# Kernel tuning notes

Hardware: AMD Instinct MI355X
Metric: run time of the kernel (lower is better)

Reference implementation:

```python
import jax, jax.numpy as jnp
import numpy as np

H = 64  # hidden_layers

def _lstm_cell(x, h, c, Wih, Whh, bih, bhh):
    # PyTorch LSTMCell: gates ordered i, f, g, o
    gates = x @ Wih.T + bih + h @ Whh.T + bhh  # (B, 4H)
    i, f, g, o = jnp.split(gates, 4, axis=-1)
    c_new = jax.nn.sigmoid(f) * c + jax.nn.sigmoid(i) * jnp.tanh(g)
    h_new = jax.nn.sigmoid(o) * jnp.tanh(c_new)
    return h_new, c_new

def setup_inputs() -> dict:
    key = jax.random.key(0)
    ks = jax.random.split(key, 12)
    B, S = 1024, 512
    s1 = 1.0 / np.sqrt(H)
    u = lambda k, shape: jax.random.uniform(k, shape, jnp.float32, -s1, s1)
    return {
        "input_t": jax.random.normal(ks[0], (B, S), jnp.float32),
        "W_ih1": u(ks[1], (4 * H, 1)),
        "W_hh1": u(ks[2], (4 * H, H)),
        "b_ih1": u(ks[3], (4 * H,)),
        "b_hh1": u(ks[4], (4 * H,)),
        "W_ih2": u(ks[5], (4 * H, H)),
        "W_hh2": u(ks[6], (4 * H, H)),
        "b_ih2": u(ks[7], (4 * H,)),
        "b_hh2": u(ks[8], (4 * H,)),
        "W_lin": u(ks[9], (1, H)),
        "b_lin": u(ks[10], (1,)),
        "future_preds": 0,
    }

def reference(input_t, W_ih1, W_hh1, b_ih1, b_hh1, W_ih2, W_hh2, b_ih2, b_hh2,
              W_lin, b_lin, future_preds):
    B = input_t.shape[0]
    z = jnp.zeros((B, H), jnp.float32)

    def step(carry, x_t):
        h1, c1, h2, c2 = carry
        h1, c1 = _lstm_cell(x_t, h1, c1, W_ih1, W_hh1, b_ih1, b_hh1)
        h2, c2 = _lstm_cell(h1, h2, c2, W_ih2, W_hh2, b_ih2, b_hh2)
        out = h2 @ W_lin.T + b_lin  # (B, 1)
        return (h1, c1, h2, c2), out[:, 0]

    xs = input_t.T[:, :, None]  # (S, B, 1)
    carry, outs = jax.lax.scan(step, (z, z, z, z), xs)
    outputs = outs.T  # (B, S)

    if future_preds > 0:  # static Python int
        def step_ar(carry_o, _):
            (h1, c1, h2, c2), out = carry_o
            h1, c1 = _lstm_cell(out, h1, c1, W_ih1, W_hh1, b_ih1, b_hh1)
            h2, c2 = _lstm_cell(h1, h2, c2, W_ih2, W_hh2, b_ih2, b_hh2)
            out = h2 @ W_lin.T + b_lin
            return ((h1, c1, h2, c2), out), out[:, 0]

        last = outs[-1][:, None]  # (B, 1)
        _, outs2 = jax.lax.scan(step_ar, (carry, last), None, length=future_preds)
        outputs = jnp.concatenate([outputs, outs2.T], axis=1)
    return outputs
```

## Files before the change

kernel.cpp:

```cpp
#include <hip/hip_runtime.h>
#include <stdint.h>

#define HD   64
#define SEQ  512
#define BTCH 1024

typedef _Float16 half2_t __attribute__((ext_vector_type(2)));

static __device__ __forceinline__ float fdot2f(uint32_t w, uint32_t hv, float acc) {
#if __has_builtin(__builtin_amdgcn_fdot2)
    half2_t a = __builtin_bit_cast(half2_t, w);
    half2_t b = __builtin_bit_cast(half2_t, hv);
    return __builtin_amdgcn_fdot2(a, b, acc, false);
#else
    half2_t a = __builtin_bit_cast(half2_t, w);
    half2_t b = __builtin_bit_cast(half2_t, hv);
    return acc + (float)a[0] * (float)b[0] + (float)a[1] * (float)b[1];
#endif
}

static __device__ __forceinline__ float rcpf_(float x) {
#if __has_builtin(__builtin_amdgcn_rcpf)
    return __builtin_amdgcn_rcpf(x);
#else
    return 1.0f / x;
#endif
}

static __device__ __forceinline__ float sigmoidf_(float x) {
    return rcpf_(1.0f + __expf(-x));
}
static __device__ __forceinline__ float tanhf_(float x) {
    float e = __expf(2.0f * x);
    return (e - 1.0f) * rcpf_(e + 1.0f);
}

static __device__ __forceinline__ uint32_t pack2h(float a, float b) {
    _Float16 ha = (_Float16)a, hb = (_Float16)b;
    uint16_t ua = __builtin_bit_cast(uint16_t, ha);
    uint16_t ub = __builtin_bit_cast(uint16_t, hb);
    return (uint32_t)ua | ((uint32_t)ub << 16);
}

static __device__ __forceinline__ uint16_t f2h(float a) {
    _Float16 ha = (_Float16)a;
    return __builtin_bit_cast(uint16_t, ha);
}

__global__ __attribute__((amdgpu_flat_work_group_size(128, 128),
                          amdgpu_waves_per_eu(2, 2)))
void lstm_kernel(
    const float* __restrict__ input,
    const float* __restrict__ Wih1,
    const float* __restrict__ Whh1,
    const float* __restrict__ bih1,
    const float* __restrict__ bhh1,
    const float* __restrict__ Wih2,
    const float* __restrict__ Whh2,
    const float* __restrict__ bih2,
    const float* __restrict__ bhh2,
    const float* __restrict__ Wlin,
    const float* __restrict__ blin,
    float* __restrict__ out)
{
    const int tid  = threadIdx.x;
    const int lane = tid & 63;
    const int gg   = tid >> 6;
    const int b    = blockIdx.x;

    const int r0 = gg * 128 + lane;
    const int r1 = r0 + 64;

    uint32_t w1a[32], w1b[32], wi2a[32], wi2b[32], wh2a[32], wh2b[32];
#pragma unroll
    for (int k = 0; k < 32; ++k) {
        w1a[k]  = pack2h(Whh1[r0 * HD + 2 * k], Whh1[r0 * HD + 2 * k + 1]);
        w1b[k]  = pack2h(Whh1[r1 * HD + 2 * k], Whh1[r1 * HD + 2 * k + 1]);
        wi2a[k] = pack2h(Wih2[r0 * HD + 2 * k], Wih2[r0 * HD + 2 * k + 1]);
        wi2b[k] = pack2h(Wih2[r1 * HD + 2 * k], Wih2[r1 * HD + 2 * k + 1]);
        wh2a[k] = pack2h(Whh2[r0 * HD + 2 * k], Whh2[r0 * HD + 2 * k + 1]);
        wh2b[k] = pack2h(Whh2[r1 * HD + 2 * k], Whh2[r1 * HD + 2 * k + 1]);
    }
    const float wx0  = Wih1[r0];
    const float wx1  = Wih1[r1];
    const float bs10 = bih1[r0] + bhh1[r0];
    const float bs11 = bih1[r1] + bhh1[r1];
    const float bs20 = bih2[r0] + bhh2[r0];
    const float bs21 = bih2[r1] + bhh2[r1];
    const float wl   = Wlin[lane];
    const float bl   = blin[0];

    __shared__ __align__(16) uint16_t hp1[2][HD];
    __shared__ __align__(16) uint16_t hp2[2][HD];
    __shared__ float g1x[4][HD];
    __shared__ float g2x[4][HD];

    hp1[gg][lane] = 0;
    hp2[gg][lane] = 0;

    float h1 = 0.f, c1 = 0.f, h2 = 0.f, c2 = 0.f;

    const float* xin = input + (size_t)b * SEQ;
    float xn = xin[0];

#pragma unroll 1
    for (int t = 0; t < SEQ; ++t) {
        const float x = xn;
        xn = xin[(t + 1) & (SEQ - 1)];

        float a0  = __builtin_fmaf(x, wx0, bs10);
        float a1  = __builtin_fmaf(x, wx1, bs11);
        float a0b = 0.f, a1b = 0.f;
        {
            const uint4* h1v = (const uint4*)(&hp1[gg][0]);
#pragma unroll
            for (int k = 0; k < 8; ++k) {
                uint4 hv = h1v[k];
                a0  = fdot2f(w1a[4 * k + 0], hv.x, a0);
                a0b = fdot2f(w1a[4 * k + 1], hv.y, a0b);
                a0  = fdot2f(w1a[4 * k + 2], hv.z, a0);
                a0b = fdot2f(w1a[4 * k + 3], hv.w, a0b);
                a1  = fdot2f(w1b[4 * k + 0], hv.x, a1);
                a1b = fdot2f(w1b[4 * k + 1], hv.y, a1b);
                a1  = fdot2f(w1b[4 * k + 2], hv.z, a1);
                a1b = fdot2f(w1b[4 * k + 3], hv.w, a1b);
            }
        }
        a0 += a0b;
        a1 += a1b;
        g1x[2 * gg + 0][lane] = a0;
        g1x[2 * gg + 1][lane] = a1;
        __syncthreads();

        {
            const float gi = gg ? g1x[0][lane] : a0;
            const float gf = gg ? g1x[1][lane] : a1;
            const float gG = gg ? a0 : g1x[2][lane];
            const float gO = gg ? a1 : g1x[3][lane];
            c1 = sigmoidf_(gf) * c1 + sigmoidf_(gi) * tanhf_(gG);
            h1 = sigmoidf_(gO) * tanhf_(c1);
        }
        hp1[gg][lane] = f2h(h1);

        float d0  = bs20;
        float d1  = bs21;
        float d0b = 0.f, d1b = 0.f;
        {
            const uint4* h1v = (const uint4*)(&hp1[gg][0]);
            const uint4* h2v = (const uint4*)(&hp2[gg][0]);
#pragma unroll
            for (int k = 0; k < 8; ++k) {
                uint4 hv = h1v[k];
                d0  = fdot2f(wi2a[4 * k + 0], hv.x, d0);
                d0b = fdot2f(wi2a[4 * k + 1], hv.y, d0b);
                d0  = fdot2f(wi2a[4 * k + 2], hv.z, d0);
                d0b = fdot2f(wi2a[4 * k + 3], hv.w, d0b);
                d1  = fdot2f(wi2b[4 * k + 0], hv.x, d1);
                d1b = fdot2f(wi2b[4 * k + 1], hv.y, d1b);
                d1  = fdot2f(wi2b[4 * k + 2], hv.z, d1);
                d1b = fdot2f(wi2b[4 * k + 3], hv.w, d1b);
                uint4 hw = h2v[k];
                d0  = fdot2f(wh2a[4 * k + 0], hw.x, d0);
                d0b = fdot2f(wh2a[4 * k + 1], hw.y, d0b);
                d0  = fdot2f(wh2a[4 * k + 2], hw.z, d0);
                d0b = fdot2f(wh2a[4 * k + 3], hw.w, d0b);
                d1  = fdot2f(wh2b[4 * k + 0], hw.x, d1);
                d1b = fdot2f(wh2b[4 * k + 1], hw.y, d1b);
                d1  = fdot2f(wh2b[4 * k + 2], hw.z, d1);
                d1b = fdot2f(wh2b[4 * k + 3], hw.w, d1b);
            }
        }
        d0 += d0b;
        d1 += d1b;
        g2x[2 * gg + 0][lane] = d0;
        g2x[2 * gg + 1][lane] = d1;
        __syncthreads();

        {
            const float gi = gg ? g2x[0][lane] : d0;
            const float gf = gg ? g2x[1][lane] : d1;
            const float gG = gg ? d0 : g2x[2][lane];
            const float gO = gg ? d1 : g2x[3][lane];
            c2 = sigmoidf_(gf) * c2 + sigmoidf_(gi) * tanhf_(gG);
            h2 = sigmoidf_(gO) * tanhf_(c2);
        }
        hp2[gg][lane] = f2h(h2);

        float r = h2 * wl;
#pragma unroll
        for (int m = 32; m >= 1; m >>= 1) r += __shfl_xor(r, m, 64);
        if (gg == 0 && lane == 0) out[(size_t)b * SEQ + t] = r + bl;
    }
}

extern "C" void kernel_launch(void* const* d_in, const int* in_sizes, int n_in,
                              void* d_out, int out_size, void* d_ws, size_t ws_size,
                              hipStream_t stream) {
    const float* input = (const float*)d_in[0];
    const float* Wih1  = (const float*)d_in[1];
    const float* Whh1  = (const float*)d_in[2];
    const float* bih1  = (const float*)d_in[3];
    const float* bhh1  = (const float*)d_in[4];
    const float* Wih2  = (const float*)d_in[5];
    const float* Whh2  = (const float*)d_in[6];
    const float* bih2  = (const float*)d_in[7];
    const float* bhh2  = (const float*)d_in[8];
    const float* Wlin  = (const float*)d_in[9];
    const float* blin  = (const float*)d_in[10];

    float* outp = (float*)d_out;

    lstm_kernel<<<dim3(BTCH), dim3(128), 0, stream>>>(
        input, Wih1, Whh1, bih1, bhh1, Wih2, Whh2, bih2, bhh2, Wlin, blin, outp);
}
```

Measured before the change: 917.0 us.

## Use four waves per block with one gate row per lane

Moves from 2 waves per block, each computing two gate rows per lane, to 4 waves per block with one gate row per lane. Each wave now does half the dot-product work per step and holds half the weight registers, which shortens the serial per-step chain and allows higher occupancy (waves_per_eu 4). In exchange, every wave redundantly computes the full cell update for all 64 hidden units. More waves also share each barrier, and the register budget per wave is tighter.

```diff
diff --git a/kernel.cpp b/kernel.cpp
--- a/kernel.cpp
+++ b/kernel.cpp
@@ -47,8 +47,8 @@
     return __builtin_bit_cast(uint16_t, ha);
 }
 
-__global__ __attribute__((amdgpu_flat_work_group_size(128, 128),
-                          amdgpu_waves_per_eu(2, 2)))
+__global__ __attribute__((amdgpu_flat_work_group_size(256, 256),
+                          amdgpu_waves_per_eu(4, 4)))
 void lstm_kernel(
     const float* __restrict__ input,
     const float* __restrict__ Wih1,
@@ -65,40 +65,33 @@
 {
     const int tid  = threadIdx.x;
     const int lane = tid & 63;
-    const int gg   = tid >> 6;
+    const int g    = tid >> 6;
     const int b    = blockIdx.x;
 
-    const int r0 = gg * 128 + lane;
-    const int r1 = r0 + 64;
+    const int row = g * HD + lane;
 
-    uint32_t w1a[32], w1b[32], wi2a[32], wi2b[32], wh2a[32], wh2b[32];
+    uint32_t w1[32], wi2[32], wh2[32];
 #pragma unroll
     for (int k = 0; k < 32; ++k) {
-        w1a[k]  = pack2h(Whh1[r0 * HD + 2 * k], Whh1[r0 * HD + 2 * k + 1]);
-        w1b[k]  = pack2h(Whh1[r1 * HD + 2 * k], Whh1[r1 * HD + 2 * k + 1]);
-        wi2a[k] = pack2h(Wih2[r0 * HD + 2 * k], Wih2[r0 * HD + 2 * k + 1]);
-        wi2b[k] = pack2h(Wih2[r1 * HD + 2 * k], Wih2[r1 * HD + 2 * k + 1]);
-        wh2a[k] = pack2h(Whh2[r0 * HD + 2 * k], Whh2[r0 * HD + 2 * k + 1]);
-        wh2b[k] = pack2h(Whh2[r1 * HD + 2 * k], Whh2[r1 * HD + 2 * k + 1]);
+        w1[k]  = pack2h(Whh1[row * HD + 2 * k], Whh1[row * HD + 2 * k + 1]);
+        wi2[k] = pack2h(Wih2[row * HD + 2 * k], Wih2[row * HD + 2 * k + 1]);
+        wh2[k] = pack2h(Whh2[row * HD + 2 * k], Whh2[row * HD + 2 * k + 1]);
     }
-    const float wx0  = Wih1[r0];
-    const float wx1  = Wih1[r1];
-    const float bs10 = bih1[r0] + bhh1[r0];
-    const float bs11 = bih1[r1] + bhh1[r1];
-    const float bs20 = bih2[r0] + bhh2[r0];
-    const float bs21 = bih2[r1] + bhh2[r1];
-    const float wl   = Wlin[lane];
-    const float bl   = blin[0];
+    const float wx  = Wih1[row];
+    const float bs1 = bih1[row] + bhh1[row];
+    const float bs2 = bih2[row] + bhh2[row];
+    const float wl  = Wlin[lane];
+    const float bl  = blin[0];
 
-    __shared__ __align__(16) uint16_t hp1[2][HD];
-    __shared__ __align__(16) uint16_t hp2[2][HD];
+    __shared__ __align__(16) uint16_t hp1[4][HD];
+    __shared__ __align__(16) uint16_t hp2[4][HD];
     __shared__ float g1x[4][HD];
     __shared__ float g2x[4][HD];
 
-    hp1[gg][lane] = 0;
-    hp2[gg][lane] = 0;
+    hp1[g][lane] = 0;
+    hp2[g][lane] = 0;
 
-    float h1 = 0.f, c1 = 0.f, h2 = 0.f, c2 = 0.f;
+    float c1 = 0.f, c2 = 0.f;
 
     const float* xin = input + (size_t)b * SEQ;
     float xn = xin[0];
@@ -108,88 +101,74 @@
         const float x = xn;
         xn = xin[(t + 1) & (SEQ - 1)];
 
-        float a0  = __builtin_fmaf(x, wx0, bs10);
-        float a1  = __builtin_fmaf(x, wx1, bs11);
-        float a0b = 0.f, a1b = 0.f;
+        float a0  = __builtin_fmaf(x, wx, bs1);
+        float a0b = 0.f;
         {
-            const uint4* h1v = (const uint4*)(&hp1[gg][0]);
+            const uint4* h1v = (const uint4*)(&hp1[g][0]);
 #pragma unroll
             for (int k = 0; k < 8; ++k) {
                 uint4 hv = h1v[k];
-                a0  = fdot2f(w1a[4 * k + 0], hv.x, a0);
-                a0b = fdot2f(w1a[4 * k + 1], hv.y, a0b);
-                a0  = fdot2f(w1a[4 * k + 2], hv.z, a0);
-                a0b = fdot2f(w1a[4 * k + 3], hv.w, a0b);
-                a1  = fdot2f(w1b[4 * k + 0], hv.x, a1);
-                a1b = fdot2f(w1b[4 * k + 1], hv.y, a1b);
-                a1  = fdot2f(w1b[4 * k + 2], hv.z, a1);
-                a1b = fdot2f(w1b[4 * k + 3], hv.w, a1b);
+                a0  = fdot2f(w1[4 * k + 0], hv.x, a0);
+                a0b = fdot2f(w1[4 * k + 1], hv.y, a0b);
+                a0  = fdot2f(w1[4 * k + 2], hv.z, a0);
+                a0b = fdot2f(w1[4 * k + 3], hv.w, a0b);
             }
         }
         a0 += a0b;
-        a1 += a1b;
-        g1x[2 * gg + 0][lane] = a0;
-        g1x[2 * gg + 1][lane] = a1;
+        g1x[g][lane] = a0;
         __syncthreads();
 
+        float h1;
         {
-            const float gi = gg ? g1x[0][lane] : a0;
-            const float gf = gg ? g1x[1][lane] : a1;
-            const float gG = gg ? a0 : g1x[2][lane];
-            const float gO = gg ? a1 : g1x[3][lane];
+            const float gi = g1x[0][lane];
+            const float gf = g1x[1][lane];
+            const float gG = g1x[2][lane];
+            const float gO = g1x[3][lane];
             c1 = sigmoidf_(gf) * c1 + sigmoidf_(gi) * tanhf_(gG);
             h1 = sigmoidf_(gO) * tanhf_(c1);
         }
-        hp1[gg][lane] = f2h(h1);
+        hp1[g][lane] = f2h(h1);
 
-        float d0  = bs20;
-        float d1  = bs21;
-        float d0b = 0.f, d1b = 0.f;
+        float d0  = bs2;
+        float d0b = 0.f;
         {
-            const uint4* h1v = (const uint4*)(&hp1[gg][0]);
-            const uint4* h2v = (const uint4*)(&hp2[gg][0]);
+            const uint4* h1v = (const uint4*)(&hp1[g][0]);
+            const uint4* h2v = (const uint4*)(&hp2[g][0]);
 #pragma unroll
             for (int k = 0; k < 8; ++k) {
                 uint4 hv = h1v[k];
-                d0  = fdot2f(wi2a[4 * k + 0], hv.x, d0);
-                d0b = fdot2f(wi2a[4 * k + 1], hv.y, d0b);
-                d0  = fdot2f(wi2a[4 * k + 2], hv.z, d0);
-                d0b = fdot2f(wi2a[4 * k + 3], hv.w, d0b);
-                d1  = fdot2f(wi2b[4 * k + 0], hv.x, d1);
-                d1b = fdot2f(wi2b[4 * k + 1], hv.y, d1b);
-                d1  = fdot2f(wi2b[4 * k + 2], hv.z, d1);
-                d1b = fdot2f(wi2b[4 * k + 3], hv.w, d1b);
+                d0  = fdot2f(wi2[4 * k + 0], hv.x, d0);
+                d0b = fdot2f(wi2[4 * k + 1], hv.y, d0b);
+                d0  = fdot2f(wi2[4 * k + 2], hv.z, d0);
+                d0b = fdot2f(wi2[4 * k + 3], hv.w, d0b);
                 uint4 hw = h2v[k];
-                d0  = fdot2f(wh2a[4 * k + 0], hw.x, d0);
-                d0b = fdot2f(wh2a[4 * k + 1], hw.y, d0b);
-                d0  = fdot2f(wh2a[4 * k + 2], hw.z, d0);
-                d0b = fdot2f(wh2a[4 * k + 3], hw.w, d0b);
-                d1  = fdot2f(wh2b[4 * k + 0], hw.x, d1);
-                d1b = fdot2f(wh2b[4 * k + 1], hw.y, d1b);
-                d1  = fdot2f(wh2b[4 * k + 2], hw.z, d1);
-                d1b = fdot2f(wh2b[4 * k + 3], hw.w, d1b);
+                d0  = fdot2f(wh2[4 * k + 0], hw.x, d0);
+                d0b = fdot2f(wh2[4 * k + 1], hw.y, d0b);
+                d0  = fdot2f(wh2[4 * k + 2], hw.z, d0);
+                d0b = fdot2f(wh2[4 * k + 3], hw.w, d0b);
             }
         }
         d0 += d0b;
-        d1 += d1b;
-        g2x[2 * gg + 0][lane] = d0;
-        g2x[2 * gg + 1][lane] = d1;
+        g2x[g][lane] = d0;
         __syncthreads();
 
+        float h2;
         {
-            const float gi = gg ? g2x[0][lane] : d0;
-            const float gf = gg ? g2x[1][lane] : d1;
-            const float gG = gg ? d0 : g2x[2][lane];
-            const float gO = gg ? d1 : g2x[3][lane];
+            const float gi = g2x[0][lane];
+            const float gf = g2x[1][lane];
+            const float gG = g2x[2][lane];
+            const float gO = g2x[3][lane];
             c2 = sigmoidf_(gf) * c2 + sigmoidf_(gi) * tanhf_(gG);
             h2 = sigmoidf_(gO) * tanhf_(c2);
         }
-        hp2[gg][lane] = f2h(h2);
+        hp2[g][lane] = f2h(h2);
 
-        float r = h2 * wl;
+        if (g == 0) {
+            float r = h2 * wl;
 #pragma unroll
-        for (int m = 32; m >= 1; m >>= 1) r += __shfl_xor(r, m, 64);
-        if (gg == 0 && lane == 0) out[(size_t)b * SEQ + t] = r + bl;
+            for (int m = 32; m >= 1; m >>= 1) r += __shfl_xor(r, m, 64);
+            if (lane == 0) out[(size_t)b * SEQ + t] = r + bl;
+        }
     }
 }
 
@@ -210,6 +189,6 @@
 
     float* outp = (float*)d_out;
 
-    lstm_kernel<<<dim3(BTCH), dim3(128), 0, stream>>>(
+    lstm_kernel<<<dim3(BTCH), dim3(256), 0, stream>>>(
         input, Wih1, Whh1, bih1, bhh1, Wih2, Whh2, bih2, bhh2, Wlin, blin, outp);
 }
```

Measured after the change: 1.025 ms. +11.8%, slower.
